# Performance work log

Hardware: AMD Instinct MI355X
Metric: run time of the kernel (lower is better)

Reference implementation:

```python
import jax, jax.numpy as jnp
import numpy as np
import math

D_MODEL = 1024
NUM_HEADS = 16


def setup_inputs() -> dict:
    key = jax.random.key(0)
    kx, kq, kk, kv, ko = jax.random.split(key, 5)
    std = math.sqrt(2.0 / (D_MODEL + D_MODEL))
    def w(k):
        return (jax.random.truncated_normal(k, -3.0, 3.0, (D_MODEL, D_MODEL), jnp.float32) * std)
    return {
        "x": jax.random.normal(kx, (2, 2048, D_MODEL), jnp.float32),
        "Wq": w(kq),
        "Wk": w(kk),
        "Wv": w(kv),
        "Wo": w(ko),
    }


def reference(x, Wq, Wk, Wv, Wo):
    B, S, D = x.shape
    H = NUM_HEADS
    dh = D // H
    # projections: weight is (d_out, d_in)
    def proj(t, W):
        y = jnp.einsum('bsd,ed->bse', t, W)
        return y.reshape(B, S, H, dh).transpose(0, 2, 1, 3)  # b h s dh
    Q = proj(x, Wq)
    K = proj(x, Wk)
    V = proj(x, Wv)
    scale = 1.0 / math.sqrt(dh)
    logits = jnp.einsum('bhqd,bhkd->bhqk', Q, K) * scale
    mask = jnp.tril(jnp.ones((S, S), dtype=bool))  # causal
    logits = jnp.where(mask, logits, -jnp.inf)
    weights = jax.nn.softmax(logits, axis=-1)
    attn = jnp.einsum('bhqk,bhkd->bhqd', weights, V)
    attn = attn.transpose(0, 2, 1, 3).reshape(B, S, D)
    return jnp.einsum('bsd,ed->bse', attn, Wo)
```

## Files before the change

### kernel.cpp

```cpp
#include <hip/hip_runtime.h>
#include <hip/hip_bf16.h>

typedef __bf16 bf16x8 __attribute__((ext_vector_type(8)));
typedef float  f32x4  __attribute__((ext_vector_type(4)));
typedef float  f32x16 __attribute__((ext_vector_type(16)));
typedef unsigned short u16x8 __attribute__((ext_vector_type(8)));
typedef unsigned short u16x4 __attribute__((ext_vector_type(4)));
typedef unsigned int   u32x4 __attribute__((ext_vector_type(4)));

#define WAITV(N) asm volatile("s_waitcnt vmcnt(" #N ")" ::: "memory")
#define SBAR()   do { __builtin_amdgcn_s_barrier(); asm volatile("" ::: "memory"); } while (0)


__device__ __forceinline__ unsigned short f2bf(float f) {
  return __builtin_bit_cast(unsigned short, (__bf16)f);
}

__device__ __forceinline__ bf16x8 ld8(const unsigned short* p) {
  return __builtin_bit_cast(bf16x8, *reinterpret_cast<const u16x8*>(p));
}

__device__ __forceinline__ unsigned int cvtpk(float a, float b) {
  unsigned int r;
  asm("v_cvt_pk_bf16_f32 %0, %1, %2" : "=v"(r) : "v"(a), "v"(b));
  return r;
}

__device__ __forceinline__ float e2(float x) {
  float r;
  asm("v_exp_f32 %0, %1" : "=v"(r) : "v"(x));
  return r;
}

__device__ __forceinline__ void gload16(const unsigned short* src, unsigned short* lds) {
  __builtin_amdgcn_global_load_lds(
      (const __attribute__((address_space(1))) unsigned int*)src,
      (__attribute__((address_space(3))) unsigned int*)lds,
      16, 0, 0);
}


__global__ __launch_bounds__(256) void cvt_inputs(
    const float* __restrict__ x, const float* __restrict__ Wq,
    const float* __restrict__ Wk, const float* __restrict__ Wv,
    const float* __restrict__ Wo,
    unsigned short* __restrict__ xb, unsigned short* __restrict__ wb) {
  const int NXC = 4194304 / 8;
  const int NWC = 1048576 / 8;
  const int total = NXC + 4 * NWC;
  for (int cid = blockIdx.x * 256 + threadIdx.x; cid < total; cid += gridDim.x * 256) {
    const float* s; unsigned short* d; int off;
    if (cid < NXC) { s = x; d = xb; off = cid * 8; }
    else {
      const int c2 = cid - NXC; const int w = c2 >> 17; const int o2 = c2 & (NWC - 1);
      s = (w == 0) ? Wq : (w == 1) ? Wk : (w == 2) ? Wv : Wo;
      d = wb + (size_t)w * 1048576;
      off = o2 * 8;
    }
    const f32x4 a  = *reinterpret_cast<const f32x4*>(s + off);
    const f32x4 b2 = *reinterpret_cast<const f32x4*>(s + off + 4);
    u16x8 o;
#pragma unroll
    for (int j = 0; j < 4; ++j) { o[j] = f2bf(a[j]); o[j + 4] = f2bf(b2[j]); }
    *reinterpret_cast<u16x8*>(d + off) = o;
  }
}


template<int BM>
__device__ __forceinline__ void gemm_body(const unsigned short* __restrict__ A,
                                          const unsigned short* __restrict__ W,
                                          void* __restrict__ Cv, int mode) {
  constexpr int FM  = BM / 32;
  constexpr int WTM = BM / 2;
  __shared__ unsigned short As[2][BM * 64];
  __shared__ unsigned short Bs[2][64 * 64];
  const int tid  = threadIdx.x;
  const int lane = tid & 63;
  const int g    = lane >> 4;
  const int lo   = lane & 15;
  const int wid  = tid >> 6;
  const int m0   = blockIdx.y * BM;
  const int n0   = blockIdx.x * 64;
  const int wm   = wid >> 1, wn = wid & 1;

  f32x4 acc[FM][2] = {};

  auto stage = [&](int buf, int k0) {
#pragma unroll
    for (int i = 0; i < BM / 32; ++i) {
      const int c   = i * 256 + tid;
      const int row = c >> 3, cc = c & 7;
      const int scc = cc ^ (row & 7);
      gload16(A + (size_t)(m0 + row) * 1024 + k0 + scc * 8, &As[buf][(i * 4 + wid) * 512]);
    }
#pragma unroll
    for (int i = 0; i < 2; ++i) {
      const int c   = i * 256 + tid;
      const int row = c >> 3, cc = c & 7;
      const int scc = cc ^ (row & 7);
      gload16(W + (size_t)(n0 + row) * 1024 + k0 + scc * 8, &Bs[buf][(i * 4 + wid) * 512]);
    }
  };

  stage(0, 0);
  stage(1, 64);
  int cur = 0;
  for (int t = 0; t < 16; ++t) {
    if (t < 15) WAITV(6); else WAITV(0);
    SBAR();
#pragma unroll
    for (int ks = 0; ks < 2; ++ks) {
      const int slot = (ks * 4 + g) ^ (lo & 7);
      bf16x8 af[FM], bvf[2];
#pragma unroll
      for (int mi = 0; mi < FM; ++mi)
        af[mi] = ld8(&As[cur][(wm * WTM + mi * 16 + lo) * 64 + slot * 8]);
#pragma unroll
      for (int ni = 0; ni < 2; ++ni)
        bvf[ni] = ld8(&Bs[cur][(wn * 32 + ni * 16 + lo) * 64 + slot * 8]);
#pragma unroll
      for (int mi = 0; mi < FM; ++mi)
#pragma unroll
        for (int ni = 0; ni < 2; ++ni)
          acc[mi][ni] = __builtin_amdgcn_mfma_f32_16x16x32_bf16(af[mi], bvf[ni], acc[mi][ni], 0, 0, 0);
    }
    SBAR();
    if (t + 2 < 16) stage(cur, (t + 2) * 64);
    cur ^= 1;
  }

#pragma unroll
  for (int mi = 0; mi < FM; ++mi) {
#pragma unroll
    for (int ni = 0; ni < 2; ++ni) {
      const int gcol = n0 + wn * 32 + ni * 16 + lo;
      if (mode == 2) {
        const int s0 = m0 + wm * WTM + mi * 16 + g * 4;
        const int b = s0 >> 11, s = s0 & 2047;
        const int h = gcol >> 6, d = gcol & 63;
        u16x4 pk;
#pragma unroll
        for (int r = 0; r < 4; ++r) pk[r] = f2bf(acc[mi][ni][r]);
        *reinterpret_cast<u16x4*>(
            &((unsigned short*)Cv)[(((size_t)(b * 16 + h)) * 64 + d) * 2048 + s]) = pk;
      } else {
#pragma unroll
        for (int r = 0; r < 4; ++r) {
          const int grow = m0 + wm * WTM + mi * 16 + g * 4 + r;
          if (mode == 0) {
            ((float*)Cv)[(size_t)grow * 1024 + gcol] = acc[mi][ni][r];
          } else {
            const unsigned short bv = f2bf(acc[mi][ni][r]);
            const int b = grow >> 11, s = grow & 2047;
            const int h = gcol >> 6, d = gcol & 63;
            ((unsigned short*)Cv)[(((size_t)(b * 16 + h)) * 2048 + s) * 64 + d] = bv;
          }
        }
      }
    }
  }
}

__global__ __launch_bounds__(256) void gemm_qkv(
    const unsigned short* __restrict__ xb,
    const unsigned short* __restrict__ wb,
    unsigned short* __restrict__ q_s,
    unsigned short* __restrict__ k_s,
    unsigned short* __restrict__ vt_s) {
  const unsigned short* W = wb + (size_t)blockIdx.z * 1048576;
  void* o; int mode;
  if (blockIdx.z == 0)      { o = q_s;  mode = 1; }
  else if (blockIdx.z == 1) { o = k_s;  mode = 1; }
  else                      { o = vt_s; mode = 2; }
  gemm_body<128>(xb, W, o, mode);
}

__global__ __launch_bounds__(256) void gemm_out(
    const unsigned short* __restrict__ a_s,
    const unsigned short* __restrict__ wb,
    float* __restrict__ out) {
  gemm_body<128>(a_s, wb + (size_t)3 * 1048576, out, 0);
}


__global__ __launch_bounds__(512, 4) void attn_fwd(
    const unsigned short* __restrict__ Q,
    const unsigned short* __restrict__ K,
    const unsigned short* __restrict__ Vt,
    unsigned short* __restrict__ O) {
  __shared__ unsigned short Kl[2][128 * 64];
  __shared__ unsigned short Vl[2][2][64 * 64];
  const int tid  = threadIdx.x;
  const int lane = tid & 63;
  const int wid  = tid >> 6;
  const int qs   = wid & 3;
  const int kh   = wid >> 2;
  const int q31  = lane & 31;
  const int hi   = lane >> 5;
  const int bi   = blockIdx.x;
  const int bh   = bi & 31;
  const int j    = (bi < 256) ? (15 - (bi >> 5)) : ((bi - 256) >> 5);
  const int b    = bh >> 4, h = bh & 15;

  const unsigned short* Qb = Q  + (size_t)bh * 2048 * 64;
  const unsigned short* Kb = K  + (size_t)bh * 2048 * 64;
  const unsigned short* Vb = Vt + (size_t)bh * 64 * 2048;
  const float SC = 0.125f * 1.4426950408889634f;

  auto stage = [&](int buf, int t) {
#pragma unroll
    for (int i = 0; i < 2; ++i) {
      const int c   = i * 512 + tid;
      const int row = c >> 3, cc = c & 7;
      const int scc = cc ^ (row & 7);
      gload16(Kb + (size_t)(t * 128 + row) * 64 + scc * 8, &Kl[buf][(i * 8 + wid) * 512]);
    }
#pragma unroll
    for (int i = 0; i < 2; ++i) {
      const int d  = tid >> 3, cc = tid & 7;
      const int scc = cc ^ (d & 7);
      gload16(Vb + (size_t)d * 2048 + t * 128 + i * 64 + scc * 8, &Vl[buf][i][wid * 512]);
    }
  };

  const int R  = j + 1;
  const int qv = j * 128 + qs * 32 + q31;

  bf16x8 qf[4];
#pragma unroll
  for (int ds = 0; ds < 4; ++ds) {
    bf16x8 tq = ld8(Qb + (size_t)qv * 64 + ds * 16 + hi * 8);
#pragma unroll
    for (int jx = 0; jx < 8; ++jx) tq[jx] = (__bf16)((float)tq[jx] * SC);
    qf[ds] = tq;
  }

  f32x16 oacc[2] = {};
  float m = -1.0e30f;
  float l = 0.f;

  stage(0, 0);
  int buf = 0;

  for (int t = 0; t < R; ++t) {
    SBAR();
    if (t + 1 < R) { stage(buf ^ 1, t + 1); WAITV(4); }
    else WAITV(0);
    SBAR();

    const bool lastt = (t == j);
    const bool skipw = lastt && (kh == 1) && (qs < 2);
    if (!skipw) {
      f32x16 sv[2];
      __builtin_amdgcn_s_setprio(1);
#pragma unroll
      for (int kt2 = 0; kt2 < 2; ++kt2) {
        const int row = kh * 64 + kt2 * 32 + q31;
        f32x16 a = {};
#pragma unroll
        for (int ds = 0; ds < 4; ++ds) {
          bf16x8 kf = ld8(&Kl[buf][row * 64 + ((ds * 2 + hi) ^ (row & 7)) * 8]);
          a = __builtin_amdgcn_mfma_f32_32x32x16_bf16(kf, qf[ds], a, 0, 0, 0);
        }
        sv[kt2] = a;
      }
      __builtin_amdgcn_s_setprio(0);

      const bool domask = lastt && !(kh == 0 && qs >= 2);
      float t0 = -1.0e30f, t1 = -1.0e30f, t2 = -1.0e30f, t3 = -1.0e30f;
      if (domask) {
#pragma unroll
        for (int kt2 = 0; kt2 < 2; ++kt2)
#pragma unroll
          for (int r = 0; r < 16; ++r) {
            float v = sv[kt2][r];
            const int key = t * 128 + kh * 64 + kt2 * 32 + (r & 3) + 8 * (r >> 2) + 4 * hi;
            if (key > qv) v = -INFINITY;
            sv[kt2][r] = v;
            if ((r & 3) == 0) t0 = fmaxf(t0, v);
            else if ((r & 3) == 1) t1 = fmaxf(t1, v);
            else if ((r & 3) == 2) t2 = fmaxf(t2, v);
            else t3 = fmaxf(t3, v);
          }
      } else {
#pragma unroll
        for (int kt2 = 0; kt2 < 2; ++kt2)
#pragma unroll
          for (int r = 0; r < 16; ++r) {
            const float v = sv[kt2][r];
            if ((r & 3) == 0) t0 = fmaxf(t0, v);
            else if ((r & 3) == 1) t1 = fmaxf(t1, v);
            else if ((r & 3) == 2) t2 = fmaxf(t2, v);
            else t3 = fmaxf(t3, v);
          }
      }
      const float tmax = fmaxf(fmaxf(t0, t1), fmaxf(t2, t3));

      if (!__all(tmax <= m + 8.f)) {
        float rmax = fmaxf(tmax, __shfl_xor(tmax, 32));
        const float mn   = fmaxf(m, rmax);
        const float corr = e2(m - mn);
        l *= corr;
#pragma unroll
        for (int dt = 0; dt < 2; ++dt)
#pragma unroll
          for (int r = 0; r < 16; ++r) oacc[dt][r] *= corr;
        m = mn;
      }

      float p0 = 0.f, p1 = 0.f, p2 = 0.f, p3 = 0.f;
#pragma unroll
      for (int kt2 = 0; kt2 < 2; ++kt2)
#pragma unroll
        for (int r = 0; r < 16; ++r) {
          const float p = e2(sv[kt2][r] - m);
          sv[kt2][r] = p;
          if ((r & 3) == 0) p0 += p;
          else if ((r & 3) == 1) p1 += p;
          else if ((r & 3) == 2) p2 += p;
          else p3 += p;
        }
      l += (p0 + p1) + (p2 + p3);

      unsigned int pw[4][4];
#pragma unroll
      for (int ks = 0; ks < 4; ++ks) {
        const int kt2 = ks >> 1, Rr = (ks & 1) * 8;
        unsigned int a0 = cvtpk(sv[kt2][Rr + 0], sv[kt2][Rr + 1]);
        unsigned int c0 = cvtpk(sv[kt2][Rr + 4], sv[kt2][Rr + 5]);
        unsigned int a1 = cvtpk(sv[kt2][Rr + 2], sv[kt2][Rr + 3]);
        unsigned int c1 = cvtpk(sv[kt2][Rr + 6], sv[kt2][Rr + 7]);
        asm("v_permlane32_swap_b32 %0, %1" : "+v"(a0), "+v"(c0));
        asm("v_permlane32_swap_b32 %0, %1" : "+v"(a1), "+v"(c1));
        pw[ks][0] = a0; pw[ks][1] = a1; pw[ks][2] = c0; pw[ks][3] = c1;
      }

      __builtin_amdgcn_s_setprio(1);
#pragma unroll
      for (int dt = 0; dt < 2; ++dt) {
        const int dl = dt * 32 + q31;
#pragma unroll
        for (int ks = 0; ks < 4; ++ks) {
          bf16x8 vfr = ld8(&Vl[buf][kh][dl * 64 + ((ks * 2 + hi) ^ (dl & 7)) * 8]);
          u32x4 t4 = {pw[ks][0], pw[ks][1], pw[ks][2], pw[ks][3]};
          bf16x8 pb = __builtin_bit_cast(bf16x8, t4);
          oacc[dt] = __builtin_amdgcn_mfma_f32_32x32x16_bf16(vfr, pb, oacc[dt], 0, 0, 0);
        }
      }
      __builtin_amdgcn_s_setprio(0);
    }

    buf ^= 1;
  }

  SBAR();
  float* VlF = (float*)&Vl[0][0][0];
  float* KlF = (float*)&Kl[0][0];
  const int mi = qs * 64 + lane;
  if (kh == 1) {
    *reinterpret_cast<f32x16*>(&VlF[mi * 32])      = oacc[0];
    *reinterpret_cast<f32x16*>(&VlF[mi * 32 + 16]) = oacc[1];
    KlF[mi * 2] = m; KlF[mi * 2 + 1] = l;
  }
  SBAR();
  if (kh == 0) {
    const f32x16 o1a = *reinterpret_cast<const f32x16*>(&VlF[mi * 32]);
    const f32x16 o1b = *reinterpret_cast<const f32x16*>(&VlF[mi * 32 + 16]);
    const float m1 = KlF[mi * 2], l1 = KlF[mi * 2 + 1];
    const float mm = fmaxf(m, m1);
    const float c0 = e2(m - mm), c1 = e2(m1 - mm);
    float lr = l * c0 + l1 * c1;
    lr += __shfl_xor(lr, 32);
    const float inv = 1.f / lr;
    const size_t obase = ((size_t)(b * 2048 + qv)) * 1024 + h * 64;
#pragma unroll
    for (int dt = 0; dt < 2; ++dt)
#pragma unroll
      for (int r4 = 0; r4 < 4; ++r4) {
        u16x4 pk;
#pragma unroll
        for (int e = 0; e < 4; ++e) {
          const int r = r4 * 4 + e;
          const float o1 = (dt == 0) ? o1a[r] : o1b[r];
          pk[e] = f2bf((oacc[dt][r] * c0 + o1 * c1) * inv);
        }
        *reinterpret_cast<u16x4*>(&O[obase + dt * 32 + r4 * 8 + hi * 4]) = pk;
      }
  }
}


extern "C" void kernel_launch(void* const* d_in, const int* in_sizes, int n_in,
                              void* d_out, int out_size, void* d_ws, size_t ws_size,
                              hipStream_t stream) {
  const float* x  = (const float*)d_in[0];
  const float* Wq = (const float*)d_in[1];
  const float* Wk = (const float*)d_in[2];
  const float* Wv = (const float*)d_in[3];
  const float* Wo = (const float*)d_in[4];
  float* out = (float*)d_out;

  char* ws = (char*)d_ws;
  const size_t MiB = 1024 * 1024;
  unsigned short* x_bf = (unsigned short*)(ws);
  unsigned short* a_s  = (unsigned short*)(ws);
  unsigned short* w_bf = (unsigned short*)(ws + 8  * MiB);
  unsigned short* q_s  = (unsigned short*)(ws + 16 * MiB);
  unsigned short* k_s  = (unsigned short*)(ws + 24 * MiB);
  unsigned short* vt_s = (unsigned short*)(ws + 32 * MiB);

  cvt_inputs<<<2048, dim3(256), 0, stream>>>(x, Wq, Wk, Wv, Wo, x_bf, w_bf);
  gemm_qkv<<<dim3(16, 32, 3), dim3(256), 0, stream>>>(x_bf, w_bf, q_s, k_s, vt_s);
  attn_fwd<<<512, dim3(512), 0, stream>>>(q_s, k_s, vt_s, a_s);
  gemm_out<<<dim3(16, 32, 1), dim3(256), 0, stream>>>(a_s, w_bf, out);
}
```

Baseline: 98.05 us.

## Fuse Q/K/V projections into one GEMM block reusing the staged x tile

Replaces the three-way z-grid QKV GEMM with a single kernel where each block loads the x tile once and multiplies it against all three weight tiles, keeping three accumulator sets. This removes redundant global and LDS loads of the activation tile. In exchange, register and shared-memory use per block roughly triples and the grid shrinks to a third, lowering parallelism. The output GEMM is de-templated but unchanged in behavior.

```diff
diff --git a/kernel.cpp b/kernel.cpp
--- a/kernel.cpp
+++ b/kernel.cpp
@@ -67,28 +67,127 @@
 }
 
 
-template<int BM>
-__device__ __forceinline__ void gemm_body(const unsigned short* __restrict__ A,
-                                          const unsigned short* __restrict__ W,
-                                          void* __restrict__ Cv, int mode) {
-  constexpr int FM  = BM / 32;
-  constexpr int WTM = BM / 2;
-  __shared__ unsigned short As[2][BM * 64];
+__global__ __launch_bounds__(256, 2) void gemm_qkv(
+    const unsigned short* __restrict__ xb,
+    const unsigned short* __restrict__ wb,
+    unsigned short* __restrict__ q_s,
+    unsigned short* __restrict__ k_s,
+    unsigned short* __restrict__ vt_s) {
+  __shared__ unsigned short As[2][128 * 64];
+  __shared__ unsigned short Bs[2][3][64 * 64];
+  const int tid  = threadIdx.x;
+  const int lane = tid & 63;
+  const int g    = lane >> 4;
+  const int lo   = lane & 15;
+  const int wid  = tid >> 6;
+  const int m0   = blockIdx.y * 128;
+  const int n0   = blockIdx.x * 64;
+  const int wm   = wid >> 1, wn = wid & 1;
+
+  f32x4 acc[3][4][2] = {};
+
+  auto stage = [&](int buf, int k0) {
+#pragma unroll
+    for (int i = 0; i < 4; ++i) {
+      const int c   = i * 256 + tid;
+      const int row = c >> 3, cc = c & 7;
+      const int scc = cc ^ (row & 7);
+      gload16(xb + (size_t)(m0 + row) * 1024 + k0 + scc * 8, &As[buf][(i * 4 + wid) * 512]);
+    }
+#pragma unroll
+    for (int w = 0; w < 3; ++w)
+#pragma unroll
+      for (int i = 0; i < 2; ++i) {
+        const int c   = i * 256 + tid;
+        const int row = c >> 3, cc = c & 7;
+        const int scc = cc ^ (row & 7);
+        gload16(wb + (size_t)w * 1048576 + (size_t)(n0 + row) * 1024 + k0 + scc * 8,
+                &Bs[buf][w][(i * 4 + wid) * 512]);
+      }
+  };
+
+  stage(0, 0);
+  stage(1, 64);
+  int cur = 0;
+  for (int t = 0; t < 16; ++t) {
+    if (t < 15) WAITV(10); else WAITV(0);
+    SBAR();
+#pragma unroll
+    for (int ks = 0; ks < 2; ++ks) {
+      const int slot = (ks * 4 + g) ^ (lo & 7);
+      bf16x8 af[4];
+#pragma unroll
+      for (int mi = 0; mi < 4; ++mi)
+        af[mi] = ld8(&As[cur][(wm * 64 + mi * 16 + lo) * 64 + slot * 8]);
+#pragma unroll
+      for (int w = 0; w < 3; ++w) {
+        bf16x8 bvf[2];
+#pragma unroll
+        for (int ni = 0; ni < 2; ++ni)
+          bvf[ni] = ld8(&Bs[cur][w][(wn * 32 + ni * 16 + lo) * 64 + slot * 8]);
+#pragma unroll
+        for (int mi = 0; mi < 4; ++mi)
+#pragma unroll
+          for (int ni = 0; ni < 2; ++ni)
+            acc[w][mi][ni] = __builtin_amdgcn_mfma_f32_16x16x32_bf16(af[mi], bvf[ni], acc[w][mi][ni], 0, 0, 0);
+      }
+    }
+    SBAR();
+    if (t + 2 < 16) stage(cur, (t + 2) * 64);
+    cur ^= 1;
+  }
+
+#pragma unroll
+  for (int w = 0; w < 3; ++w) {
+    unsigned short* Cv = (w == 0) ? q_s : (w == 1) ? k_s : vt_s;
+#pragma unroll
+    for (int mi = 0; mi < 4; ++mi) {
+#pragma unroll
+      for (int ni = 0; ni < 2; ++ni) {
+        const int gcol = n0 + wn * 32 + ni * 16 + lo;
+        const int h = gcol >> 6, d = gcol & 63;
+        if (w == 2) {
+          const int s0 = m0 + wm * 64 + mi * 16 + g * 4;
+          const int b = s0 >> 11, s = s0 & 2047;
+          u16x4 pk;
+#pragma unroll
+          for (int r = 0; r < 4; ++r) pk[r] = f2bf(acc[w][mi][ni][r]);
+          *reinterpret_cast<u16x4*>(&Cv[(((size_t)(b * 16 + h)) * 64 + d) * 2048 + s]) = pk;
+        } else {
+#pragma unroll
+          for (int r = 0; r < 4; ++r) {
+            const int grow = m0 + wm * 64 + mi * 16 + g * 4 + r;
+            const int b = grow >> 11, s = grow & 2047;
+            Cv[(((size_t)(b * 16 + h)) * 2048 + s) * 64 + d] = f2bf(acc[w][mi][ni][r]);
+          }
+        }
+      }
+    }
+  }
+}
+
+
+__global__ __launch_bounds__(256) void gemm_out(
+    const unsigned short* __restrict__ A,
+    const unsigned short* __restrict__ wb,
+    float* __restrict__ out) {
+  const unsigned short* W = wb + (size_t)3 * 1048576;
+  __shared__ unsigned short As[2][128 * 64];
   __shared__ unsigned short Bs[2][64 * 64];
   const int tid  = threadIdx.x;
   const int lane = tid & 63;
   const int g    = lane >> 4;
   const int lo   = lane & 15;
   const int wid  = tid >> 6;
-  const int m0   = blockIdx.y * BM;
+  const int m0   = blockIdx.y * 128;
   const int n0   = blockIdx.x * 64;
   const int wm   = wid >> 1, wn = wid & 1;
 
-  f32x4 acc[FM][2] = {};
+  f32x4 acc[4][2] = {};
 
   auto stage = [&](int buf, int k0) {
 #pragma unroll
-    for (int i = 0; i < BM / 32; ++i) {
+    for (int i = 0; i < 4; ++i) {
       const int c   = i * 256 + tid;
       const int row = c >> 3, cc = c & 7;
       const int scc = cc ^ (row & 7);
@@ -112,15 +211,15 @@
 #pragma unroll
     for (int ks = 0; ks < 2; ++ks) {
       const int slot = (ks * 4 + g) ^ (lo & 7);
-      bf16x8 af[FM], bvf[2];
-#pragma unroll
-      for (int mi = 0; mi < FM; ++mi)
-        af[mi] = ld8(&As[cur][(wm * WTM + mi * 16 + lo) * 64 + slot * 8]);
+      bf16x8 af[4], bvf[2];
+#pragma unroll
+      for (int mi = 0; mi < 4; ++mi)
+        af[mi] = ld8(&As[cur][(wm * 64 + mi * 16 + lo) * 64 + slot * 8]);
 #pragma unroll
       for (int ni = 0; ni < 2; ++ni)
         bvf[ni] = ld8(&Bs[cur][(wn * 32 + ni * 16 + lo) * 64 + slot * 8]);
 #pragma unroll
-      for (int mi = 0; mi < FM; ++mi)
+      for (int mi = 0; mi < 4; ++mi)
 #pragma unroll
         for (int ni = 0; ni < 2; ++ni)
           acc[mi][ni] = __builtin_amdgcn_mfma_f32_16x16x32_bf16(af[mi], bvf[ni], acc[mi][ni], 0, 0, 0);
@@ -131,56 +230,16 @@
   }
 
 #pragma unroll
-  for (int mi = 0; mi < FM; ++mi) {
+  for (int mi = 0; mi < 4; ++mi)
 #pragma unroll
     for (int ni = 0; ni < 2; ++ni) {
       const int gcol = n0 + wn * 32 + ni * 16 + lo;
-      if (mode == 2) {
-        const int s0 = m0 + wm * WTM + mi * 16 + g * 4;
-        const int b = s0 >> 11, s = s0 & 2047;
-        const int h = gcol >> 6, d = gcol & 63;
-        u16x4 pk;
-#pragma unroll
-        for (int r = 0; r < 4; ++r) pk[r] = f2bf(acc[mi][ni][r]);
-        *reinterpret_cast<u16x4*>(
-            &((unsigned short*)Cv)[(((size_t)(b * 16 + h)) * 64 + d) * 2048 + s]) = pk;
-      } else {
-#pragma unroll
-        for (int r = 0; r < 4; ++r) {
-          const int grow = m0 + wm * WTM + mi * 16 + g * 4 + r;
-          if (mode == 0) {
-            ((float*)Cv)[(size_t)grow * 1024 + gcol] = acc[mi][ni][r];
-          } else {
-            const unsigned short bv = f2bf(acc[mi][ni][r]);
-            const int b = grow >> 11, s = grow & 2047;
-            const int h = gcol >> 6, d = gcol & 63;
-            ((unsigned short*)Cv)[(((size_t)(b * 16 + h)) * 2048 + s) * 64 + d] = bv;
-          }
-        }
-      }
-    }
-  }
-}
-
-__global__ __launch_bounds__(256) void gemm_qkv(
-    const unsigned short* __restrict__ xb,
-    const unsigned short* __restrict__ wb,
-    unsigned short* __restrict__ q_s,
-    unsigned short* __restrict__ k_s,
-    unsigned short* __restrict__ vt_s) {
-  const unsigned short* W = wb + (size_t)blockIdx.z * 1048576;
-  void* o; int mode;
-  if (blockIdx.z == 0)      { o = q_s;  mode = 1; }
-  else if (blockIdx.z == 1) { o = k_s;  mode = 1; }
-  else                      { o = vt_s; mode = 2; }
-  gemm_body<128>(xb, W, o, mode);
-}
-
-__global__ __launch_bounds__(256) void gemm_out(
-    const unsigned short* __restrict__ a_s,
-    const unsigned short* __restrict__ wb,
-    float* __restrict__ out) {
-  gemm_body<128>(a_s, wb + (size_t)3 * 1048576, out, 0);
+#pragma unroll
+      for (int r = 0; r < 4; ++r) {
+        const int grow = m0 + wm * 64 + mi * 16 + g * 4 + r;
+        out[(size_t)grow * 1024 + gcol] = acc[mi][ni][r];
+      }
+    }
 }
 
 
@@ -411,7 +470,7 @@
   unsigned short* vt_s = (unsigned short*)(ws + 32 * MiB);
 
   cvt_inputs<<<2048, dim3(256), 0, stream>>>(x, Wq, Wk, Wv, Wo, x_bf, w_bf);
-  gemm_qkv<<<dim3(16, 32, 3), dim3(256), 0, stream>>>(x_bf, w_bf, q_s, k_s, vt_s);
+  gemm_qkv<<<dim3(16, 32), dim3(256), 0, stream>>>(x_bf, w_bf, q_s, k_s, vt_s);
   attn_fwd<<<512, dim3(512), 0, stream>>>(q_s, k_s, vt_s, a_s);
-  gemm_out<<<dim3(16, 32, 1), dim3(256), 0, stream>>>(a_s, w_bf, out);
-}
+  gemm_out<<<dim3(16, 32), dim3(256), 0, stream>>>(a_s, w_bf, out);
+}
```

After: 89.38 us (median of 2 runs). -8.8%, faster.
